# Kernel optimization log

Hardware: AMD Instinct MI355X
Metric: run time of the kernel (lower is better)

## Reference

```python
import jax, jax.numpy as jnp
import numpy as np

N, DIM, HID, NCLS, E = 100000, 256, 16, 64, 3200000
NEG_SLOPE = 0.2


def setup_inputs() -> dict:
    key = jax.random.key(0)
    ks = jax.random.split(key, 10)
    x = jax.random.normal(ks[0], (N, DIM), dtype=jnp.float32)
    edge_index = jax.random.randint(ks[1], (2, E), 0, N, dtype=jnp.int64)
    # GATConv params (heads=1): glorot-ish scaled normals
    W1 = jax.random.normal(ks[2], (DIM, HID), dtype=jnp.float32) / np.sqrt(DIM)
    a_src1 = jax.random.normal(ks[3], (HID,), dtype=jnp.float32) / np.sqrt(HID)
    a_dst1 = jax.random.normal(ks[4], (HID,), dtype=jnp.float32) / np.sqrt(HID)
    b1 = jnp.zeros((HID,), dtype=jnp.float32)
    W2 = jax.random.normal(ks[5], (HID, NCLS), dtype=jnp.float32) / np.sqrt(HID)
    a_src2 = jax.random.normal(ks[6], (NCLS,), dtype=jnp.float32) / np.sqrt(NCLS)
    a_dst2 = jax.random.normal(ks[7], (NCLS,), dtype=jnp.float32) / np.sqrt(NCLS)
    b2 = jnp.zeros((NCLS,), dtype=jnp.float32)
    return {"x": x, "edge_index": edge_index, "W1": W1, "a_src1": a_src1,
            "a_dst1": a_dst1, "b1": b1, "W2": W2, "a_src2": a_src2,
            "a_dst2": a_dst2, "b2": b2}


def gat_conv(x, src, dst, W, a_s, a_d, b, n):
    # PyG GATConv, heads=1: h = x W; e_ij = LeakyReLU(a_s.h_j + a_d.h_i)
    h = x @ W                                   # [N, out]
    alpha_s = h @ a_s                           # [N]
    alpha_d = h @ a_d                           # [N]
    e = jax.nn.leaky_relu(alpha_s[src] + alpha_d[dst], NEG_SLOPE)  # [E]
    # softmax over edges grouped by destination node
    m = jax.ops.segment_max(e, dst, num_segments=n)
    m = jnp.where(jnp.isfinite(m), m, 0.0)
    ee = jnp.exp(e - m[dst])
    denom = jax.ops.segment_sum(ee, dst, num_segments=n)
    alpha = ee / denom[dst]                     # self-loops guarantee denom > 0
    out = jax.ops.segment_sum(h[src] * alpha[:, None], dst, num_segments=n)
    return out + b


def reference(x, edge_index, W1, a_src1, a_dst1, b1, W2, a_src2, a_dst2, b2):
    n = x.shape[0]
    loop = jnp.arange(n, dtype=edge_index.dtype)
    src = jnp.concatenate([edge_index[0], loop])  # add self-loops (PyG default)
    dst = jnp.concatenate([edge_index[1], loop])
    h = jax.nn.relu(gat_conv(x, src, dst, W1, a_src1, a_dst1, b1, n))
    # F.dropout treated as identity (inference / deterministic reference)
    out = gat_conv(h, src, dst, W2, a_src2, a_dst2, b2, n)
    return jax.nn.log_softmax(out, axis=1)
```

## Files before the change

kernel.cpp:

```cpp
#include <hip/hip_runtime.h>
#include <hip/hip_fp16.h>


#define DIM 256
#define HID 16
#define NCLS 64
#define NEG 0.2f
#define P1_CHUNK 2048
#define KITER 8
#define CAP 8704

typedef _Float16 f16x8 __attribute__((ext_vector_type(8)));
typedef float f32x4 __attribute__((ext_vector_type(4)));

__device__ __forceinline__ float lrelu(float v) { return v >= 0.f ? v : NEG * v; }

__device__ __forceinline__ uint4 pack_half8(const float* v) {
    __half2 p0 = __floats2half2_rn(v[0], v[1]);
    __half2 p1 = __floats2half2_rn(v[2], v[3]);
    __half2 p2 = __floats2half2_rn(v[4], v[5]);
    __half2 p3 = __floats2half2_rn(v[6], v[7]);
    return make_uint4(*(unsigned*)&p0, *(unsigned*)&p1, *(unsigned*)&p2, *(unsigned*)&p3);
}

__device__ __forceinline__ void unpack_half8(uint4 u, float* f) {
    float2 f0 = __half22float2(*(__half2*)&u.x);
    float2 f1 = __half22float2(*(__half2*)&u.y);
    float2 f2 = __half22float2(*(__half2*)&u.z);
    float2 f3 = __half22float2(*(__half2*)&u.w);
    f[0] = f0.x; f[1] = f0.y; f[2] = f1.x; f[3] = f1.y;
    f[4] = f2.x; f[5] = f2.y; f[6] = f3.x; f[7] = f3.y;
}

__global__ void vsd_kernel(const float* __restrict__ W2, const float* __restrict__ as2,
                           const float* __restrict__ ad2, float* __restrict__ vsd,
                           int* __restrict__ bkt_cnt, int* __restrict__ bkt_cur, int capb) {
    int t = threadIdx.x;
    bkt_cnt[t] = 0;
    bkt_cur[t] = capb ? t * capb : 0;
    if (t < 32) {
        int j = t & 15;
        const float* a = (t < 16) ? as2 : ad2;
        float s = 0.f;
        for (int c = 0; c < NCLS; ++c) s += W2[j * NCLS + c] * a[c];
        vsd[t] = s;
    }
}


__global__ __launch_bounds__(256) void p0_hist(const int* __restrict__ dst, int E,
                                               int* __restrict__ bkt_cnt) {
    __shared__ int hist[512];
    int t = threadIdx.x;
    for (int i = t; i < 512; i += 256) hist[i] = 0;
    __syncthreads();
    int base = blockIdx.x * P1_CHUNK;
#pragma unroll
    for (int k = 0; k < KITER; ++k) {
        int idx = base + k * 256 + t;
        if (idx < E) atomicAdd(&hist[dst[idx] >> 8], 1);
    }
    __syncthreads();
    for (int i = t; i < 512; i += 256)
        if (hist[i]) atomicAdd(&bkt_cnt[i], hist[i]);
}

__global__ void scanb(int* __restrict__ bkt_cnt, int* __restrict__ bkt_cur,
                      int* __restrict__ bkt_base, int nb, int capb) {
    __shared__ int lds[512];
    int t = threadIdx.x;
    int v = 0;
    if (t < nb) v = capb ? (bkt_cur[t] - t * capb) : bkt_cnt[t];
    lds[t] = v;
    __syncthreads();
    for (int o = 1; o < 512; o <<= 1) {
        int x = (t >= o) ? lds[t - o] : 0;
        __syncthreads();
        lds[t] += x;
        __syncthreads();
    }
    if (t < nb) {
        int e = lds[t] - v;
        bkt_base[t] = e;
        if (capb) bkt_cnt[t] = v;
        else bkt_cur[t] = e;
    }
}

struct H1S {
    _Float16 w1t[16][264];
    _Float16 hst[4][16][16];
};

__global__ __launch_bounds__(256) void p1h1_kernel(
    const int* __restrict__ ei, int E, int* __restrict__ bkt_cur,
    int* __restrict__ coarse, int nS, int h1blk, int capb,
    const float* __restrict__ x, const float* __restrict__ W1,
    const float* __restrict__ asw, const float* __restrict__ adw,
    uint4* __restrict__ h1h, float* __restrict__ as1, float* __restrict__ ad1, int n) {
    __shared__ union __align__(16) { int hist[512]; H1S h1; } sm;
    int t = threadIdx.x;
    int bid = blockIdx.x;
    int total = nS + h1blk;
    int f0 = (int)(((long long)bid * h1blk) / total);
    int f1 = (int)(((long long)(bid + 1) * h1blk) / total);
    if (f1 == f0) {
        int sb = bid - f0;
        int base = sb * P1_CHUNK;
        int sarr[KITER], darr[KITER];
        for (int i = t; i < 512; i += 256) sm.hist[i] = 0;
#pragma unroll
        for (int k = 0; k < KITER; ++k) {
            int idx = base + k * 256 + t;
            if (idx < E) {
                sarr[k] = ei[idx];
                darr[k] = ei[E + idx];
            } else {
                darr[k] = -1;
            }
        }
        __syncthreads();
#pragma unroll
        for (int k = 0; k < KITER; ++k)
            if (darr[k] >= 0) atomicAdd(&sm.hist[darr[k] >> 8], 1);
        __syncthreads();
        for (int b = t; b < 512; b += 256) {
            int c = sm.hist[b];
            sm.hist[b] = c ? atomicAdd(&bkt_cur[b], c) : 0;
        }
        __syncthreads();
#pragma unroll
        for (int k = 0; k < KITER; ++k) {
            int d = darr[k];
            if (d >= 0) {
                int bk = d >> 8;
                int pos = atomicAdd(&sm.hist[bk], 1);
                if (capb) pos = min(pos, (bk + 1) * capb - 1);
                coarse[pos] = (sarr[k] << 8) | (d & 255);
            }
        }
    } else {
        int hb = f0;
        {
            const float* row = W1 + t * HID;
#pragma unroll
            for (int nn2 = 0; nn2 < 16; ++nn2)
                sm.h1.w1t[nn2][t] = (_Float16)row[nn2];
        }
        __syncthreads();
        int lane = t & 63, wave = t >> 6;
        int q = lane >> 4, nn = lane & 15;
        float asv = asw[nn], adv = adw[nn];
#pragma unroll
        for (int it = 0; it < 4; ++it) {
            int nb = hb * 256 + wave * 64 + it * 16;
            int node = nb + nn;
            const float* xr = x + (size_t)min(node, n - 1) * DIM;
            float4 st[16];
#pragma unroll
            for (int s = 0; s < 8; ++s) {
                int kb = s * 32 + q * 8;
                st[2 * s]     = *(const float4*)(xr + kb);
                st[2 * s + 1] = *(const float4*)(xr + kb + 4);
            }
            f32x4 acc = {0.f, 0.f, 0.f, 0.f};
#pragma unroll
            for (int s = 0; s < 8; ++s) {
                int kb = s * 32 + q * 8;
                f16x8 bf = *(const f16x8*)&sm.h1.w1t[nn][kb];
                float4 a0 = st[2 * s], a1 = st[2 * s + 1];
                f16x8 af;
                af[0] = (_Float16)a0.x; af[1] = (_Float16)a0.y;
                af[2] = (_Float16)a0.z; af[3] = (_Float16)a0.w;
                af[4] = (_Float16)a1.x; af[5] = (_Float16)a1.y;
                af[6] = (_Float16)a1.z; af[7] = (_Float16)a1.w;
                acc = __builtin_amdgcn_mfma_f32_16x16x32_f16(af, bf, acc, 0, 0, 0);
            }
            if (nb < n) {
#pragma unroll
                for (int r = 0; r < 4; ++r) {
                    float v = acc[r];
                    sm.h1.hst[wave][q * 4 + r][nn] = (_Float16)v;
                    float t1 = v * asv, t2 = v * adv;
#pragma unroll
                    for (int mm = 1; mm < 16; mm <<= 1) {
                        t1 += __shfl_xor(t1, mm, 64);
                        t2 += __shfl_xor(t2, mm, 64);
                    }
                    if (nn == 0) {
                        int nd = nb + q * 4 + r;
                        if (nd < n) { as1[nd] = t1; ad1[nd] = t2; }
                    }
                }
                __builtin_amdgcn_s_waitcnt(0);
                if (lane < 32) {
                    int nl = lane >> 1, jq = lane & 1;
                    int nd = nb + nl;
                    if (nd < n)
                        h1h[(size_t)nd * 2 + jq] = *(const uint4*)&sm.h1.hst[wave][nl][jq * 8];
                }
            }
        }
    }
}

__global__ __launch_bounds__(256) void p2_fine(const int* __restrict__ coarse,
                                               const int* __restrict__ bkt_base,
                                               const int* __restrict__ bkt_cnt,
                                               int* __restrict__ csr, int* __restrict__ row_ptr,
                                               int* __restrict__ deg, int n, int capb) {
    __shared__ int cnt[256];
    __shared__ int off[256];
    __shared__ int csr_loc[CAP];
    int b = blockIdx.x;
    int t = threadIdx.x;
    cnt[t] = 0;
    __syncthreads();
    int wbase = bkt_base[b];
    int rbase = capb ? b * capb : wbase;
    int m = bkt_cnt[b];
    for (int i = t; i < m; i += 256) atomicAdd(&cnt[coarse[rbase + i] & 255], 1);
    __syncthreads();
    int v = cnt[t];
    off[t] = v;
    __syncthreads();
    for (int o = 1; o < 256; o <<= 1) {
        int xg = (t >= o) ? off[t - o] : 0;
        __syncthreads();
        off[t] += xg;
        __syncthreads();
    }
    int excl = off[t] - v;
    int node = b * 256 + t;
    if (node < n) {
        row_ptr[node] = wbase + excl;
        deg[node] = v;
    }
    __syncthreads();
    cnt[t] = excl;
    __syncthreads();
    if (m <= CAP) {
        for (int i = t; i < m; i += 256) {
            int rec = coarse[rbase + i];
            int pos = atomicAdd(&cnt[rec & 255], 1);
            csr_loc[pos] = rec >> 8;
        }
        __syncthreads();
        for (int i = t; i < m; i += 256) csr[wbase + i] = csr_loc[i];
    } else {
        for (int i = t; i < m; i += 256) {
            int rec = coarse[rbase + i];
            int pos = atomicAdd(&cnt[rec & 255], 1);
            csr[wbase + pos] = rec >> 8;
        }
    }
}


__device__ __forceinline__ void agg_core(
    const uint4* __restrict__ hh, const float* __restrict__ as, float adi,
    int node, int start, int cnt, const int* __restrict__ csr,
    int lg, int eq, int jq, int gbase, float* acc, float& denomv) {
    float w0 = __expf(lrelu(as[node] + adi));
    float w0s = (eq == 0) ? w0 : 0.f;
    float hs[8];
    unpack_half8(hh[(size_t)node * 2 + jq], hs);
#pragma unroll
    for (int i = 0; i < 8; ++i) acc[i] = w0s * hs[i];
    float denom = w0s;
    for (int q0 = 0; q0 < cnt; q0 += 16) {
        int myq = q0 + lg;
        int sv = 0;
        float wv = 0.f;
        if (myq < cnt) {
            sv = csr[start + myq];
            wv = __expf(lrelu(as[sv] + adi));
        }
#pragma unroll
        for (int r = 0; r < 2; ++r) {
            int lane = gbase + r * 8 + eq;
            int s = __shfl(sv, lane, 64);
            float w = __shfl(wv, lane, 64);
            denom += w;
            float hf[8];
            unpack_half8(hh[(size_t)s * 2 + jq], hf);
#pragma unroll
            for (int i = 0; i < 8; ++i) acc[i] += w * hf[i];
        }
    }
#pragma unroll
    for (int m = 2; m <= 8; m <<= 1) {
#pragma unroll
        for (int i = 0; i < 8; ++i) acc[i] += __shfl_xor(acc[i], m, 64);
        denom += __shfl_xor(denom, m, 64);
    }
    denomv = denom;
}

__global__ __launch_bounds__(256) void agg1_kernel(
    const uint4* __restrict__ hh, const float* __restrict__ as, const float* __restrict__ ad,
    const int* __restrict__ row_ptr, const int* __restrict__ deg, const int* __restrict__ csr,
    const float* __restrict__ bias, const float* __restrict__ vsd,
    uint4* __restrict__ outh, float* __restrict__ as_out, float* __restrict__ ad_out,
    int n) {
    int t = threadIdx.x;
    int node = blockIdx.x * 16 + (t >> 4);
    if (node >= n) return;
    int lg = t & 15, jq = lg & 1, eq = lg >> 1, gbase = t & 48;
    float adi = ad[node];
    float acc[8];
    float denom;
    agg_core(hh, as, adi, node, row_ptr[node], deg[node], csr, lg, eq, jq, gbase, acc, denom);
    float inv = 1.f / denom;
    const float* bj = bias + jq * 8;
    float val[8];
#pragma unroll
    for (int i = 0; i < 8; ++i) val[i] = fmaxf(acc[i] * inv + bj[i], 0.f);
    if (eq == 0) outh[(size_t)node * 2 + jq] = pack_half8(val);
    const float* vs = vsd + jq * 8;
    const float* vd = vsd + 16 + jq * 8;
    float t1 = 0.f, t2 = 0.f;
#pragma unroll
    for (int i = 0; i < 8; ++i) { t1 += val[i] * vs[i]; t2 += val[i] * vd[i]; }
    t1 += __shfl_xor(t1, 1, 64);
    t2 += __shfl_xor(t2, 1, 64);
    if (lg == 0) { as_out[node] = t1; ad_out[node] = t2; }
}

__global__ __launch_bounds__(256) void agg2_final_kernel(
    const uint4* __restrict__ hh, const float* __restrict__ as, const float* __restrict__ ad,
    const int* __restrict__ row_ptr, const int* __restrict__ deg, const int* __restrict__ csr,
    const float* __restrict__ W2, const float* __restrict__ b2,
    float* __restrict__ out, int n) {
    __shared__ float a2s[16 * HID];
    __shared__ float w2s[HID * NCLS];
    __shared__ float b2s[NCLS];
    int t = threadIdx.x;
    for (int i = t; i < HID * NCLS; i += 256) w2s[i] = W2[i];
    if (t < NCLS) b2s[t] = b2[t];
    int g = t >> 4;
    int node = blockIdx.x * 16 + g;
    int lg = t & 15, jq = lg & 1, eq = lg >> 1, gbase = t & 48;
    if (node < n) {
        float adi = ad[node];
        float acc[8];
        float denom;
        agg_core(hh, as, adi, node, row_ptr[node], deg[node], csr, lg, eq, jq, gbase, acc, denom);
        float inv = 1.f / denom;
        if (eq == 0) {
            float* dst = &a2s[g * HID + jq * 8];
            *(float4*)dst = make_float4(acc[0] * inv, acc[1] * inv, acc[2] * inv, acc[3] * inv);
            *(float4*)(dst + 4) = make_float4(acc[4] * inv, acc[5] * inv, acc[6] * inv, acc[7] * inv);
        }
    }
    __syncthreads();
    int wv = t >> 6;
    int c = t & 63;
#pragma unroll
    for (int i = 0; i < 4; ++i) {
        int nl = i * 4 + wv;
        int gn = blockIdx.x * 16 + nl;
        if (gn >= n) continue;
        const float* ar = &a2s[nl * HID];
        float v = b2s[c];
#pragma unroll
        for (int j = 0; j < HID; ++j) v += ar[j] * w2s[j * NCLS + c];
        float mx = v;
#pragma unroll
        for (int off = 1; off < 64; off <<= 1) mx = fmaxf(mx, __shfl_xor(mx, off, 64));
        float ex = __expf(v - mx);
        float s = ex;
#pragma unroll
        for (int off = 1; off < 64; off <<= 1) s += __shfl_xor(s, off, 64);
        out[(size_t)gn * NCLS + c] = (v - mx) - __logf(s);
    }
}

extern "C" void kernel_launch(void* const* d_in, const int* in_sizes, int n_in,
                              void* d_out, int out_size, void* d_ws, size_t ws_size,
                              hipStream_t stream) {
    const float* x    = (const float*)d_in[0];
    const int*   ei   = (const int*)d_in[1];
    const float* W1   = (const float*)d_in[2];
    const float* a_s1 = (const float*)d_in[3];
    const float* a_d1 = (const float*)d_in[4];
    const float* b1   = (const float*)d_in[5];
    const float* W2   = (const float*)d_in[6];
    const float* a_s2 = (const float*)d_in[7];
    const float* a_d2 = (const float*)d_in[8];
    const float* b2   = (const float*)d_in[9];
    float* out = (float*)d_out;

    const int N = in_sizes[0] / DIM;
    const int E = in_sizes[1] / 2;
    const int NB = (N + 255) >> 8;
    const int nS = (E + P1_CHUNK - 1) / P1_CHUNK;
    const int h1blk = (N + 255) / 256;

    char* p = (char*)d_ws;
    auto alloc = [&](size_t bytes) {
        char* r = p;
        p += (bytes + 255) & ~(size_t)255;
        return r;
    };
    int*   bkt_cnt  = (int*)alloc(512 * 4);
    int*   bkt_base = (int*)alloc(512 * 4);
    int*   bkt_cur  = (int*)alloc(512 * 4);
    int*   csr      = (int*)alloc((size_t)E * 4);
    int*   row_ptr  = (int*)alloc((size_t)N * 4);
    int*   deg      = (int*)alloc((size_t)N * 4);
    float* as1      = (float*)alloc((size_t)N * 4);
    float* ad1      = (float*)alloc((size_t)N * 4);
    float* as2      = (float*)alloc((size_t)N * 4);
    float* ad2      = (float*)alloc((size_t)N * 4);
    float* vsd      = (float*)alloc(32 * 4);
    uint4* h1h      = (uint4*)alloc((size_t)N * 32);
    uint4* hreluh   = (uint4*)alloc((size_t)N * 32);

    int capb = 10240;
    size_t used = (size_t)(p - (char*)d_ws);
    size_t pad_bytes = (size_t)512 * capb * 4;
    int* coarse;
    if (ws_size - used >= pad_bytes) {
        coarse = (int*)alloc(pad_bytes);
    } else {
        capb = 0;
        coarse = (int*)alloc((size_t)E * 4);
    }

    vsd_kernel<<<1, 512, 0, stream>>>(W2, a_s2, a_d2, vsd, bkt_cnt, bkt_cur, capb);
    if (!capb) {
        p0_hist<<<nS, 256, 0, stream>>>(ei + E, E, bkt_cnt);
        scanb<<<1, 512, 0, stream>>>(bkt_cnt, bkt_cur, bkt_base, NB, 0);
    }
    p1h1_kernel<<<nS + h1blk, 256, 0, stream>>>(ei, E, bkt_cur, coarse, nS, h1blk, capb,
                                                x, W1, a_s1, a_d1, h1h, as1, ad1, N);
    if (capb)
        scanb<<<1, 512, 0, stream>>>(bkt_cnt, bkt_cur, bkt_base, NB, capb);
    p2_fine<<<NB, 256, 0, stream>>>(coarse, bkt_base, bkt_cnt, csr, row_ptr, deg, N, capb);
    agg1_kernel<<<(N + 15) / 16, 256, 0, stream>>>(h1h, as1, ad1, row_ptr, deg, csr,
                                                   b1, vsd, hreluh, as2, ad2, N);
    agg2_final_kernel<<<(N + 15) / 16, 256, 0, stream>>>(hreluh, as2, ad2, row_ptr, deg, csr,
                                                         W2, b2, out, N);
}
```

Baseline: 326.3 us.

## Vectorize edge loads, fold bucket scan into p2_fine, prefetch CSR in aggregation

After: 304.9 us. 6.6% less time.

```diff
diff --git a/kernel.cpp b/kernel.cpp
--- a/kernel.cpp
+++ b/kernel.cpp
@@ -6,12 +6,14 @@
 #define HID 16
 #define NCLS 64
 #define NEG 0.2f
-#define P1_CHUNK 2048
-#define KITER 8
+#define P1_CHUNK 4096
+#define KITER 16
 #define CAP 8704
 
 typedef _Float16 f16x8 __attribute__((ext_vector_type(8)));
 typedef float f32x4 __attribute__((ext_vector_type(4)));
+
+#define PIN4(v) asm volatile("" : "+v"(v.x), "+v"(v.y), "+v"(v.z), "+v"(v.w))
 
 __device__ __forceinline__ float lrelu(float v) { return v >= 0.f ? v : NEG * v; }
 
@@ -66,11 +68,10 @@
 }
 
 __global__ void scanb(int* __restrict__ bkt_cnt, int* __restrict__ bkt_cur,
-                      int* __restrict__ bkt_base, int nb, int capb) {
+                      int* __restrict__ bkt_base, int nb) {
     __shared__ int lds[512];
     int t = threadIdx.x;
-    int v = 0;
-    if (t < nb) v = capb ? (bkt_cur[t] - t * capb) : bkt_cnt[t];
+    int v = (t < nb) ? bkt_cnt[t] : 0;
     lds[t] = v;
     __syncthreads();
     for (int o = 1; o < 512; o <<= 1) {
@@ -82,8 +83,7 @@
     if (t < nb) {
         int e = lds[t] - v;
         bkt_base[t] = e;
-        if (capb) bkt_cnt[t] = v;
-        else bkt_cur[t] = e;
+        bkt_cur[t] = e;
     }
 }
 
@@ -109,14 +109,24 @@
         int base = sb * P1_CHUNK;
         int sarr[KITER], darr[KITER];
         for (int i = t; i < 512; i += 256) sm.hist[i] = 0;
-#pragma unroll
-        for (int k = 0; k < KITER; ++k) {
-            int idx = base + k * 256 + t;
-            if (idx < E) {
-                sarr[k] = ei[idx];
-                darr[k] = ei[E + idx];
+        bool e4 = ((E & 3) == 0);
+#pragma unroll
+        for (int k = 0; k < KITER / 4; ++k) {
+            int idx = base + (k * 256 + t) * 4;
+            if (e4 && idx + 3 < E) {
+                int4 s4 = *(const int4*)&ei[idx];
+                int4 d4 = *(const int4*)&ei[E + idx];
+                sarr[4 * k] = s4.x; sarr[4 * k + 1] = s4.y;
+                sarr[4 * k + 2] = s4.z; sarr[4 * k + 3] = s4.w;
+                darr[4 * k] = d4.x; darr[4 * k + 1] = d4.y;
+                darr[4 * k + 2] = d4.z; darr[4 * k + 3] = d4.w;
             } else {
-                darr[k] = -1;
+#pragma unroll
+                for (int j = 0; j < 4; ++j) {
+                    int id2 = idx + j;
+                    if (id2 < E) { sarr[4 * k + j] = ei[id2]; darr[4 * k + j] = ei[E + id2]; }
+                    else darr[4 * k + j] = -1;
+                }
             }
         }
         __syncthreads();
@@ -151,7 +161,7 @@
         int lane = t & 63, wave = t >> 6;
         int q = lane >> 4, nn = lane & 15;
         float asv = asw[nn], adv = adw[nn];
-#pragma unroll
+#pragma unroll 1
         for (int it = 0; it < 4; ++it) {
             int nb = hb * 256 + wave * 64 + it * 16;
             int node = nb + nn;
@@ -163,6 +173,8 @@
                 st[2 * s]     = *(const float4*)(xr + kb);
                 st[2 * s + 1] = *(const float4*)(xr + kb + 4);
             }
+#pragma unroll
+            for (int i = 0; i < 16; ++i) PIN4(st[i]);
             f32x4 acc = {0.f, 0.f, 0.f, 0.f};
 #pragma unroll
             for (int s = 0; s < 8; ++s) {
@@ -204,9 +216,10 @@
     }
 }
 
-__global__ __launch_bounds__(256) void p2_fine(const int* __restrict__ coarse,
+__global__ __launch_bounds__(512) void p2_fine(const int* __restrict__ coarse,
                                                const int* __restrict__ bkt_base,
                                                const int* __restrict__ bkt_cnt,
+                                               const int* __restrict__ bkt_cur,
                                                int* __restrict__ csr, int* __restrict__ row_ptr,
                                                int* __restrict__ deg, int n, int capb) {
     __shared__ int cnt[256];
@@ -214,41 +227,59 @@
     __shared__ int csr_loc[CAP];
     int b = blockIdx.x;
     int t = threadIdx.x;
-    cnt[t] = 0;
-    __syncthreads();
-    int wbase = bkt_base[b];
+    int m, wbase;
+    if (capb) {
+        int* sc = csr_loc;
+        int cv = bkt_cur[t] - t * capb;
+        sc[t] = cv;
+        __syncthreads();
+        for (int o = 1; o < 512; o <<= 1) {
+            int xg = (t >= o) ? sc[t - o] : 0;
+            __syncthreads();
+            sc[t] += xg;
+            __syncthreads();
+        }
+        m = bkt_cur[b] - b * capb;
+        wbase = sc[b] - m;
+        __syncthreads();
+    } else {
+        m = bkt_cnt[b];
+        wbase = bkt_base[b];
+    }
     int rbase = capb ? b * capb : wbase;
-    int m = bkt_cnt[b];
-    for (int i = t; i < m; i += 256) atomicAdd(&cnt[coarse[rbase + i] & 255], 1);
-    __syncthreads();
-    int v = cnt[t];
-    off[t] = v;
+    if (t < 256) cnt[t] = 0;
+    __syncthreads();
+    for (int i = t; i < m; i += 512) atomicAdd(&cnt[coarse[rbase + i] & 255], 1);
+    __syncthreads();
+    int v = 0;
+    if (t < 256) { v = cnt[t]; off[t] = v; }
     __syncthreads();
     for (int o = 1; o < 256; o <<= 1) {
-        int xg = (t >= o) ? off[t - o] : 0;
-        __syncthreads();
-        off[t] += xg;
-        __syncthreads();
-    }
-    int excl = off[t] - v;
-    int node = b * 256 + t;
-    if (node < n) {
-        row_ptr[node] = wbase + excl;
-        deg[node] = v;
-    }
-    __syncthreads();
-    cnt[t] = excl;
+        int xg = (t >= o && t < 256) ? off[t - o] : 0;
+        __syncthreads();
+        if (t < 256) off[t] += xg;
+        __syncthreads();
+    }
+    if (t < 256) {
+        int excl = off[t] - v;
+        int node = b * 256 + t;
+        if (node < n) {
+            row_ptr[node] = wbase + excl;
+            deg[node] = v;
+        }
+        cnt[t] = excl;
+    }
     __syncthreads();
     if (m <= CAP) {
-        for (int i = t; i < m; i += 256) {
+        for (int i = t; i < m; i += 512) {
             int rec = coarse[rbase + i];
             int pos = atomicAdd(&cnt[rec & 255], 1);
             csr_loc[pos] = rec >> 8;
         }
         __syncthreads();
-        for (int i = t; i < m; i += 256) csr[wbase + i] = csr_loc[i];
+        for (int i = t; i < m; i += 512) csr[wbase + i] = csr_loc[i];
     } else {
-        for (int i = t; i < m; i += 256) {
+        for (int i = t; i < m; i += 512) {
             int rec = coarse[rbase + i];
             int pos = atomicAdd(&cnt[rec & 255], 1);
             csr[wbase + pos] = rec >> 8;
@@ -268,25 +299,27 @@
 #pragma unroll
     for (int i = 0; i < 8; ++i) acc[i] = w0s * hs[i];
     float denom = w0s;
+    int sv = (lg < cnt) ? csr[start + lg] : 0;
+    float av = as[sv];
     for (int q0 = 0; q0 < cnt; q0 += 16) {
-        int myq = q0 + lg;
-        int sv = 0;
-        float wv = 0.f;
-        if (myq < cnt) {
-            sv = csr[start + myq];
-            wv = __expf(lrelu(as[sv] + adi));
-        }
-#pragma unroll
-        for (int r = 0; r < 2; ++r) {
-            int lane = gbase + r * 8 + eq;
-            int s = __shfl(sv, lane, 64);
-            float w = __shfl(wv, lane, 64);
-            denom += w;
-            float hf[8];
-            unpack_half8(hh[(size_t)s * 2 + jq], hf);
-#pragma unroll
-            for (int i = 0; i < 8; ++i) acc[i] += w * hf[i];
-        }
+        int nq = q0 + 16 + lg;
+        int nsv = (nq < cnt) ? csr[start + nq] : 0;
+        float nav = as[nsv];
+        float wv = (q0 + lg < cnt) ? __expf(lrelu(av + adi)) : 0.f;
+        int s0 = __shfl(sv, gbase + eq, 64);
+        int s1 = __shfl(sv, gbase + 8 + eq, 64);
+        float wA = __shfl(wv, gbase + eq, 64);
+        float wB = __shfl(wv, gbase + 8 + eq, 64);
+        uint4 u0 = hh[(size_t)s0 * 2 + jq];
+        uint4 u1 = hh[(size_t)s1 * 2 + jq];
+        denom += wA + wB;
+        float h0[8], h1v[8];
+        unpack_half8(u0, h0);
+        unpack_half8(u1, h1v);
+#pragma unroll
+        for (int i = 0; i < 8; ++i) acc[i] += wA * h0[i] + wB * h1v[i];
+        sv = nsv;
+        av = nav;
     }
 #pragma unroll
     for (int m = 2; m <= 8; m <<= 1) {
@@ -431,13 +464,12 @@
     vsd_kernel<<<1, 512, 0, stream>>>(W2, a_s2, a_d2, vsd, bkt_cnt, bkt_cur, capb);
     if (!capb) {
         p0_hist<<<nS, 256, 0, stream>>>(ei + E, E, bkt_cnt);
-        scanb<<<1, 512, 0, stream>>>(bkt_cnt, bkt_cur, bkt_base, NB, 0);
+        scanb<<<1, 512, 0, stream>>>(bkt_cnt, bkt_cur, bkt_base, NB);
     }
     p1h1_kernel<<<nS + h1blk, 256, 0, stream>>>(ei, E, bkt_cur, coarse, nS, h1blk, capb,
                                                 x, W1, a_s1, a_d1, h1h, as1, ad1, N);
-    if (capb)
-        scanb<<<1, 512, 0, stream>>>(bkt_cnt, bkt_cur, bkt_base, NB, capb);
-    p2_fine<<<NB, 256, 0, stream>>>(coarse, bkt_base, bkt_cnt, csr, row_ptr, deg, N, capb);
+    p2_fine<<<NB, 512, 0, stream>>>(coarse, bkt_base, bkt_cnt, bkt_cur,
+                                    csr, row_ptr, deg, N, capb);
     agg1_kernel<<<(N + 15) / 16, 256, 0, stream>>>(h1h, as1, ad1, row_ptr, deg, csr,
                                                    b1, vsd, hreluh, as2, ad2, N);
     agg2_final_kernel<<<(N + 15) / 16, 256, 0, stream>>>(hreluh, as2, ad2, row_ptr, deg, csr,
```
